# Kernel optimization log

Measured on AMD Instinct MI355X. Metric: run time of the kernel, lower is better.

Reference implementation:

```python
import jax, jax.numpy as jnp
import numpy as np

DIM = 1024
HEADS = 16
HIDDEN = 4 * DIM


def layernorm(x, g, b, eps=1e-5):
    mu = jnp.mean(x, axis=-1, keepdims=True)
    var = jnp.mean(jnp.square(x - mu), axis=-1, keepdims=True)
    return (x - mu) * jax.lax.rsqrt(var + eps) * g + b


def setup_inputs() -> dict:
    key = jax.random.key(0)
    ks = jax.random.split(key, 8)
    s = DIM ** -0.5
    return {
        "x": jax.random.normal(ks[0], (2, 2048, DIM), dtype=jnp.float32),
        "ln1_g": jnp.ones((DIM,), jnp.float32),
        "ln1_b": jnp.zeros((DIM,), jnp.float32),
        "qkv_w": jax.random.normal(ks[1], (DIM, 3 * DIM), jnp.float32) * s,
        "proj_w": jax.random.normal(ks[2], (DIM, DIM), jnp.float32) * s,
        "proj_b": jnp.zeros((DIM,), jnp.float32),
        "ln2_g": jnp.ones((DIM,), jnp.float32),
        "ln2_b": jnp.zeros((DIM,), jnp.float32),
        "fc1_w": jax.random.normal(ks[3], (DIM, HIDDEN), jnp.float32) * s,
        "fc1_b": jnp.zeros((HIDDEN,), jnp.float32),
        "fc2_w": jax.random.normal(ks[4], (HIDDEN, DIM), jnp.float32) * (HIDDEN ** -0.5),
        "fc2_b": jnp.zeros((DIM,), jnp.float32),
    }


def block_fwd(x, ln1_g, ln1_b, qkv_w, proj_w, proj_b, ln2_g, ln2_b,
              fc1_w, fc1_b, fc2_w, fc2_b):
    B, N, C = x.shape
    H = HEADS
    Dh = C // H
    scale = Dh ** -0.5
    # --- attention branch (pre-norm) ---
    h = layernorm(x, ln1_g, ln1_b)
    qkv = h @ qkv_w                     # [B,N,3C] (no bias: qkv_bias=False)
    qkv = qkv.reshape(B, N, 3, H, Dh)
    q = qkv[:, :, 0].transpose(0, 2, 1, 3)   # [B,H,N,Dh]
    k = qkv[:, :, 1].transpose(0, 2, 1, 3)
    v = qkv[:, :, 2].transpose(0, 2, 1, 3)
    attn = jnp.einsum('bhqd,bhkd->bhqk', q, k) * scale
    attn = jax.nn.softmax(attn, axis=-1)
    o = jnp.einsum('bhqk,bhkd->bhqd', attn, v)
    o = o.transpose(0, 2, 1, 3).reshape(B, N, C)
    x = x + (o @ proj_w + proj_b)
    # --- MLP branch (pre-norm) ---
    h = layernorm(x, ln2_g, ln2_b)
    h = jax.nn.gelu(h @ fc1_w + fc1_b, approximate=False)  # torch nn.GELU = exact erf
    x = x + (h @ fc2_w + fc2_b)
    return x


def reference(x, ln1_g, ln1_b, qkv_w, proj_w, proj_b, ln2_g, ln2_b,
              fc1_w, fc1_b, fc2_w, fc2_b):
    return block_fwd(x, ln1_g, ln1_b, qkv_w, proj_w, proj_b, ln2_g, ln2_b,
                     fc1_w, fc1_b, fc2_w, fc2_b)
```

## Files before the change

kernel.cpp:

```cpp
#include <hip/hip_runtime.h>
#include <math.h>

typedef unsigned short u16;
typedef unsigned int u32;
typedef __attribute__((ext_vector_type(8))) short short8;
typedef __attribute__((ext_vector_type(4))) float f32x4;
typedef __attribute__((ext_vector_type(16))) float f32x16;
typedef __attribute__((ext_vector_type(2))) u32 u32x2;
typedef __attribute__((ext_vector_type(4))) u32 u32x4;
typedef __attribute__((ext_vector_type(4))) u16 u16x4;

typedef __attribute__((address_space(1))) const void gmem_t;
typedef __attribute__((address_space(3))) void lmem_t;

__device__ __forceinline__ u16 f2bf(float f) {
  u32 u = __builtin_bit_cast(u32, f);
  u = u + 0x7fffu + ((u >> 16) & 1u);
  return (u16)(u >> 16);
}

__device__ __forceinline__ u32 cvt_pk_bf16(float a, float b) {
  u32 r;
  asm("v_cvt_pk_bf16_f32 %0, %1, %2" : "=v"(r) : "v"(a), "v"(b));
  return r;
}

__device__ __forceinline__ void g2l16(const void* g, void* l) {
  __builtin_amdgcn_global_load_lds((gmem_t*)g, (lmem_t*)l, 16, 0, 0);
}

template <int N> __device__ __forceinline__ void waitcnt_vm() {
  if constexpr (N == 0)      asm volatile("s_waitcnt vmcnt(0)" ::: "memory");
  else if constexpr (N == 4) asm volatile("s_waitcnt vmcnt(4)" ::: "memory");
  else if constexpr (N == 6) asm volatile("s_waitcnt vmcnt(6)" ::: "memory");
  else if constexpr (N == 8) asm volatile("s_waitcnt vmcnt(8)" ::: "memory");
  else static_assert(N == 0 || N == 4 || N == 6 || N == 8, "add literal");
}

#define QSCALE 0.1803368801111204f

__global__ __launch_bounds__(256) void wtrans_all(
    const float* __restrict__ qkvw, const float* __restrict__ projw,
    const float* __restrict__ fc1w, const float* __restrict__ fc2w,
    u16* __restrict__ o_qkv, u16* __restrict__ o_proj,
    u16* __restrict__ o_fc1, u16* __restrict__ o_fc2) {
  int id = (int)blockIdx.x;
  const float* in; u16* out; int R, C, bid;
  if (id < 768)       { in = qkvw;  out = o_qkv;  R = 1024; C = 3072; bid = id; }
  else if (id < 1024) { in = projw; out = o_proj; R = 1024; C = 1024; bid = id - 768; }
  else if (id < 2048) { in = fc1w;  out = o_fc1;  R = 1024; C = 4096; bid = id - 1024; }
  else                { in = fc2w;  out = o_fc2;  R = 4096; C = 1024; bid = id - 2048; }
  __shared__ float t[64][65];
  int tid = threadIdx.x;
  int nbx = C >> 6;
  int bx = bid % nbx, by = bid / nbx;
  int r0 = by << 6, c0 = bx << 6;
  int lr = tid >> 2, lc = (tid & 3) << 4;
  const float* src = in + (size_t)(r0 + lr) * C + c0 + lc;
#pragma unroll
  for (int j = 0; j < 4; ++j) {
    f32x4 v = *(const f32x4*)(src + j * 4);
    t[lr][lc + j * 4 + 0] = v.x; t[lr][lc + j * 4 + 1] = v.y;
    t[lr][lc + j * 4 + 2] = v.z; t[lr][lc + j * 4 + 3] = v.w;
  }
  __syncthreads();
  int oc = tid >> 2, orr = (tid & 3) << 4;
  u16* dst = out + (size_t)(c0 + oc) * R + r0 + orr;
  u32 u[8];
#pragma unroll
  for (int j = 0; j < 8; ++j)
    u[j] = (u32)f2bf(t[orr + 2 * j][oc]) | ((u32)f2bf(t[orr + 2 * j + 1][oc]) << 16);
  u32x4 v0; v0.x = u[0]; v0.y = u[1]; v0.z = u[2]; v0.w = u[3];
  u32x4 v1; v1.x = u[4]; v1.y = u[5]; v1.z = u[6]; v1.w = u[7];
  *(u32x4*)(dst) = v0;
  *(u32x4*)(dst + 8) = v1;
}

__global__ __launch_bounds__(256) void lnorm(const float* __restrict__ in,
                                             const float* __restrict__ gw,
                                             const float* __restrict__ bw,
                                             u16* __restrict__ out) {
  int r = blockIdx.x, tid = threadIdx.x;
  const f32x4 v = *((const f32x4*)(in + (size_t)r * 1024) + tid);
  float s = v.x + v.y + v.z + v.w;
  float ss = v.x * v.x + v.y * v.y + v.z * v.z + v.w * v.w;
#pragma unroll
  for (int o = 32; o >= 1; o >>= 1) { s += __shfl_xor(s, o); ss += __shfl_xor(ss, o); }
  __shared__ float red[8];
  int w = tid >> 6;
  if ((tid & 63) == 0) { red[w] = s; red[4 + w] = ss; }
  __syncthreads();
  s = red[0] + red[1] + red[2] + red[3];
  ss = red[4] + red[5] + red[6] + red[7];
  float mu = s * (1.0f / 1024.0f);
  float var = ss * (1.0f / 1024.0f) - mu * mu;
  float rstd = rsqrtf(var + 1e-5f);
  const f32x4 g4 = *((const f32x4*)gw + tid);
  const f32x4 b4 = *((const f32x4*)bw + tid);
  u16x4 o;
  o.x = f2bf((v.x - mu) * rstd * g4.x + b4.x);
  o.y = f2bf((v.y - mu) * rstd * g4.y + b4.y);
  o.z = f2bf((v.z - mu) * rstd * g4.z + b4.z);
  o.w = f2bf((v.w - mu) * rstd * g4.w + b4.w);
  *((u16x4*)(out + (size_t)r * 1024) + tid) = o;
}

template <int EPI, int BM, int BN>
__global__ __launch_bounds__(256, 2) void gemm_bt(
    const u16* __restrict__ A, const u16* __restrict__ BT, int M, int N, int K,
    const float* __restrict__ bias, const float* __restrict__ resid,
    float* __restrict__ fout, u16* __restrict__ bout) {
  constexpr int AIT = BM / 32, BIT = BN / 32;
  constexpr int L = AIT + BIT;
  constexpr int MR = BM / 32, NR = BN / 32;
  __shared__ __align__(16) u16 smA[2][BM * 64];
  __shared__ __align__(16) u16 smB[2][BN * 64];
  int tid = threadIdx.x;
  int w = tid >> 6, l = tid & 63, lq = l & 15, g = l >> 4;
  int nbx = N / BN;
  int t = (int)blockIdx.x;
  int cpx = (int)gridDim.x >> 3;
  t = (t & 7) * cpx + (t >> 3);
  int by = t / nbx, bx = t - by * nbx;
  long brow = (long)by * BM, bcol = (long)bx * BN;
  int wr = w >> 1, wc = w & 1;

  const u16* aS[AIT]; const u16* bS[BIT];
#pragma unroll
  for (int it = 0; it < AIT; ++it) {
    int p = it * 256 + tid;
    int row = p >> 3;
    int gc = (p & 7) ^ (row & 7);
    aS[it] = A + (size_t)(brow + row) * K + gc * 8;
  }
#pragma unroll
  for (int it = 0; it < BIT; ++it) {
    int p = it * 256 + tid;
    int row = p >> 3;
    int gc = (p & 7) ^ (row & 7);
    bS[it] = BT + (size_t)(bcol + row) * K + gc * 8;
  }
  auto STAGE = [&](int buf, int k0) {
#pragma unroll
    for (int it = 0; it < AIT; ++it) g2l16(aS[it] + k0, &smA[buf][it * 2048 + w * 512]);
#pragma unroll
    for (int it = 0; it < BIT; ++it) g2l16(bS[it] + k0, &smB[buf][it * 2048 + w * 512]);
  };

  f32x4 zero = {0.f, 0.f, 0.f, 0.f};
  f32x4 acc[MR][NR];
#pragma unroll
  for (int m = 0; m < MR; ++m)
#pragma unroll
    for (int n = 0; n < NR; ++n) acc[m][n] = zero;

  int NT = K >> 6;
  STAGE(0, 0);
  for (int tt = 0; tt < NT; ++tt) {
    int cur = tt & 1;
    int knext = ((tt + 1) == NT ? 0 : (tt + 1)) << 6;
    STAGE(cur ^ 1, knext);
    waitcnt_vm<L>();
    __builtin_amdgcn_s_barrier();
    asm volatile("" ::: "memory");

    const char* sA = (const char*)&smA[cur][0];
    const char* sB = (const char*)&smB[cur][0];
#pragma unroll
    for (int c = 0; c < 2; ++c) {
      short8 af[MR], bfb[NR];
#pragma unroll
      for (int m = 0; m < MR; ++m) {
        int r = wr * (BM / 2) + m * 16 + lq;
        af[m] = *(const short8*)(sA + r * 128 + ((g * 16 + c * 64) ^ ((r & 7) << 4)));
      }
#pragma unroll
      for (int n = 0; n < NR; ++n) {
        int r = wc * (BN / 2) + n * 16 + lq;
        bfb[n] = *(const short8*)(sB + r * 128 + ((g * 16 + c * 64) ^ ((r & 7) << 4)));
      }
#pragma unroll
      for (int m = 0; m < MR; ++m)
#pragma unroll
        for (int n = 0; n < NR; ++n)
          acc[m][n] = __builtin_amdgcn_mfma_f32_16x16x32_bf16(af[m], bfb[n], acc[m][n], 0, 0, 0);
    }
    asm volatile("" ::: "memory");
    __builtin_amdgcn_s_barrier();
  }
  waitcnt_vm<0>();

  long colbase = bcol + wc * (BN / 2);
#pragma unroll
  for (int m = 0; m < MR; ++m) {
#pragma unroll
    for (int n = 0; n < NR; ++n) {
      f32x4 v = acc[m][n];
      long col = colbase + n * 16 + lq;
      long row0 = brow + wr * (BM / 2) + m * 16 + g * 4;
      float bb = bias[col];
#pragma unroll
      for (int i = 0; i < 4; ++i) {
        long idx = (row0 + i) * N + col;
        fout[idx] = resid[idx] + v[i] + bb;
      }
    }
  }
}

template <int EPI>
__global__ __launch_bounds__(256, 4) void gemm32(
    const u16* __restrict__ A, const u16* __restrict__ BT, int M, int N, int K,
    const float* __restrict__ bias,
    u16* __restrict__ bout, u16* __restrict__ bout2, u16* __restrict__ bout3) {
  __shared__ __align__(16) u16 smA[2][128 * 32];
  __shared__ __align__(16) u16 smB[2][128 * 32];
  int tid = threadIdx.x;
  int w = tid >> 6, l = tid & 63, lq = l & 15, g = l >> 4;
  int nbx = N >> 7;
  int t = (int)blockIdx.x;
  int cpx = (int)gridDim.x >> 3;
  t = (t & 7) * cpx + (t >> 3);
  int by = t / nbx, bx = t - by * nbx;
  long brow = (long)by << 7, bcol = (long)bx << 7;
  int wr = w >> 1, wc = w & 1;

  const u16* aS[2]; const u16* bS[2];
#pragma unroll
  for (int it = 0; it < 2; ++it) {
    int p = it * 256 + tid;
    int sp = (p & 7) ^ ((p >> 3) & 7);
    int row = ((p >> 3) << 1) | (sp >> 2);
    int c = sp & 3;
    aS[it] = A + (size_t)(brow + row) * K + c * 8;
    bS[it] = BT + (size_t)(bcol + row) * K + c * 8;
  }
  auto STAGE = [&](int buf, int k0) {
#pragma unroll
    for (int it = 0; it < 2; ++it) {
      g2l16(aS[it] + k0, &smA[buf][it * 2048 + w * 512]);
      g2l16(bS[it] + k0, &smB[buf][it * 2048 + w * 512]);
    }
  };

  f32x4 zero = {0.f, 0.f, 0.f, 0.f};
  f32x4 acc[4][4];
#pragma unroll
  for (int m = 0; m < 4; ++m)
#pragma unroll
    for (int n = 0; n < 4; ++n) acc[m][n] = zero;

  int NT = K >> 5;
  STAGE(0, 0);
  for (int tt = 0; tt < NT; ++tt) {
    int cur = tt & 1;
    int knext = ((tt + 1) == NT ? 0 : (tt + 1)) << 5;
    STAGE(cur ^ 1, knext);
    waitcnt_vm<4>();
    __builtin_amdgcn_s_barrier();
    asm volatile("" ::: "memory");

    const char* sA = (const char*)&smA[cur][0];
    const char* sB = (const char*)&smB[cur][0];
    short8 af[4], bfb[4];
#pragma unroll
    for (int m = 0; m < 4; ++m) {
      int r = wr * 64 + m * 16 + lq;
      af[m] = *(const short8*)(sA + ((r >> 1) * 128 +
                ((((r & 1) << 6) + (g << 4)) ^ (((r >> 1) & 7) << 4))));
    }
#pragma unroll
    for (int n = 0; n < 4; ++n) {
      int r = wc * 64 + n * 16 + lq;
      bfb[n] = *(const short8*)(sB + ((r >> 1) * 128 +
                ((((r & 1) << 6) + (g << 4)) ^ (((r >> 1) & 7) << 4))));
    }
    __builtin_amdgcn_s_setprio(1);
#pragma unroll
    for (int m = 0; m < 4; ++m)
#pragma unroll
      for (int n = 0; n < 4; ++n)
        acc[m][n] = __builtin_amdgcn_mfma_f32_16x16x32_bf16(af[m], bfb[n], acc[m][n], 0, 0, 0);
    __builtin_amdgcn_s_setprio(0);
    asm volatile("" ::: "memory");
    __builtin_amdgcn_s_barrier();
  }
  waitcnt_vm<0>();

#pragma unroll
  for (int m = 0; m < 4; ++m) {
#pragma unroll
    for (int n = 0; n < 4; ++n) {
      f32x4 v = acc[m][n];
      long col = bcol + wc * 64 + n * 16 + lq;
      long row0 = brow + wr * 64 + m * 16 + g * 4;
      if constexpr (EPI == 0) {
        int part = (int)(bcol >> 10);
        long colq = col - ((long)part << 10);
        int hh = (int)(colq >> 6), d = (int)(colq & 63);
#pragma unroll
        for (int i = 0; i < 4; ++i) {
          long row = row0 + i;
          long b = row >> 11, nq = row & 2047;
          long bh = b * 16 + hh;
          if (part == 0)      bout [(bh * 2048 + nq) * 64 + d] = f2bf(v[i] * QSCALE);
          else if (part == 1) bout2[(bh * 2048 + nq) * 64 + d] = f2bf(v[i]);
          else                bout3[(bh * 64 + d) * 2048 + nq] = f2bf(v[i]);
        }
      } else {
        float bb = bias[col];
#pragma unroll
        for (int i = 0; i < 4; ++i) {
          float xg = v[i] + bb;
          float ge = 0.5f * xg * (1.0f + erff(xg * 0.70710678118654752f));
          bout[(row0 + i) * (long)N + col] = f2bf(ge);
        }
      }
    }
  }
}

template <int BASE>
__device__ __forceinline__ short8 mk_pfrag(const f32x16& s) {
  u32 x = cvt_pk_bf16(exp2f(s[BASE + 0]), exp2f(s[BASE + 1]));
  u32 y = cvt_pk_bf16(exp2f(s[BASE + 2]), exp2f(s[BASE + 3]));
  u32 u = cvt_pk_bf16(exp2f(s[BASE + 4]), exp2f(s[BASE + 5]));
  u32 v = cvt_pk_bf16(exp2f(s[BASE + 6]), exp2f(s[BASE + 7]));
  asm("v_permlane32_swap_b32 %0, %1" : "+v"(x), "+v"(u));
  asm("v_permlane32_swap_b32 %0, %1" : "+v"(y), "+v"(v));
  u32x4 f; f.x = x; f.y = y; f.z = u; f.w = v;
  return __builtin_bit_cast(short8, f);
}

__global__ __launch_bounds__(256, 2) void attn_fwd(const u16* __restrict__ qb,
                                                   const u16* __restrict__ kbuf,
                                                   const u16* __restrict__ vtb,
                                                   u16* __restrict__ ob) {
  __shared__ __align__(16) u16 kl[2][64 * 64];
  __shared__ __align__(16) u16 vl[2][64 * 64];
  int tid = threadIdx.x;
  int w = tid >> 6, l = tid & 63, q32 = l & 31, hi = l >> 5;
  int bh = (int)blockIdx.x & 31;
  int qt = (int)blockIdx.x >> 5;

  const u16* qp = qb + ((size_t)bh * 2048 + qt * 128 + w * 32 + q32) * 64 + hi * 8;
  short8 qf[4];
#pragma unroll
  for (int kc = 0; kc < 4; ++kc) qf[kc] = *(const short8*)(qp + kc * 16);

  const u16* kS[2]; const u16* vS[2];
#pragma unroll
  for (int it = 0; it < 2; ++it) {
    int p = it * 256 + tid;
    int row = p >> 3;
    int gc = (p & 7) ^ (row & 7);
    kS[it] = kbuf + ((size_t)bh * 2048 + row) * 64 + gc * 8;
    vS[it] = vtb + ((size_t)bh * 64 + row) * 2048 + gc * 8;
  }
  auto issue = [&](int buf, int kt0) {
#pragma unroll
    for (int it = 0; it < 2; ++it) {
      g2l16(kS[it] + (size_t)kt0 * 64, &kl[buf][it * 2048 + w * 512]);
      g2l16(vS[it] + kt0,              &vl[buf][it * 2048 + w * 512]);
    }
  };

  f32x16 z16 = {0,0,0,0,0,0,0,0,0,0,0,0,0,0,0,0};
  f32x16 accO0 = z16, accO1 = z16, accl = z16;
  u32x4 ov; ov.x = ov.y = ov.z = ov.w = 0x3F803F80u;
  short8 onesf = __builtin_bit_cast(short8, ov);
  int swz = (q32 & 7) << 4;

  issue(0, 0);
  for (int t = 0; t < 32; ++t) {
    int cur = t & 1;
    issue(cur ^ 1, ((t + 1) & 31) << 6);
    waitcnt_vm<4>();
    __builtin_amdgcn_s_barrier();
    asm volatile("" ::: "memory");

    const char* klc = (const char*)&kl[cur][0];
    const char* vlc = (const char*)&vl[cur][0];

    f32x16 s0 = z16, s1 = z16;
    __builtin_amdgcn_s_setprio(1);
#pragma unroll
    for (int kc = 0; kc < 4; ++kc) {
      short8 k0 = *(const short8*)(klc + (q32 * 128 +        ((kc * 32 + hi * 16) ^ swz)));
      short8 k1 = *(const short8*)(klc + ((32 + q32) * 128 + ((kc * 32 + hi * 16) ^ swz)));
      s0 = __builtin_amdgcn_mfma_f32_32x32x16_bf16(k0, qf[kc], s0, 0, 0, 0);
      s1 = __builtin_amdgcn_mfma_f32_32x32x16_bf16(k1, qf[kc], s1, 0, 0, 0);
    }
    __builtin_amdgcn_s_setprio(0);

    short8 pf0 = mk_pfrag<0>(s0);
    short8 pf1 = mk_pfrag<8>(s0);
    short8 pf2 = mk_pfrag<0>(s1);
    short8 pf3 = mk_pfrag<8>(s1);

    short8 va0[4], va1[4];
#pragma unroll
    for (int c = 0; c < 4; ++c) {
      va0[c] = *(const short8*)(vlc + (q32 * 128 +        ((c * 32 + hi * 16) ^ swz)));
      va1[c] = *(const short8*)(vlc + ((32 + q32) * 128 + ((c * 32 + hi * 16) ^ swz)));
    }
    __builtin_amdgcn_s_setprio(1);
    accO0 = __builtin_amdgcn_mfma_f32_32x32x16_bf16(va0[0], pf0, accO0, 0, 0, 0);
    accO1 = __builtin_amdgcn_mfma_f32_32x32x16_bf16(va1[0], pf0, accO1, 0, 0, 0);
    accl  = __builtin_amdgcn_mfma_f32_32x32x16_bf16(onesf,  pf0, accl,  0, 0, 0);
    accO0 = __builtin_amdgcn_mfma_f32_32x32x16_bf16(va0[1], pf1, accO0, 0, 0, 0);
    accO1 = __builtin_amdgcn_mfma_f32_32x32x16_bf16(va1[1], pf1, accO1, 0, 0, 0);
    accl  = __builtin_amdgcn_mfma_f32_32x32x16_bf16(onesf,  pf1, accl,  0, 0, 0);
    accO0 = __builtin_amdgcn_mfma_f32_32x32x16_bf16(va0[2], pf2, accO0, 0, 0, 0);
    accO1 = __builtin_amdgcn_mfma_f32_32x32x16_bf16(va1[2], pf2, accO1, 0, 0, 0);
    accl  = __builtin_amdgcn_mfma_f32_32x32x16_bf16(onesf,  pf2, accl,  0, 0, 0);
    accO0 = __builtin_amdgcn_mfma_f32_32x32x16_bf16(va0[3], pf3, accO0, 0, 0, 0);
    accO1 = __builtin_amdgcn_mfma_f32_32x32x16_bf16(va1[3], pf3, accO1, 0, 0, 0);
    accl  = __builtin_amdgcn_mfma_f32_32x32x16_bf16(onesf,  pf3, accl,  0, 0, 0);
    __builtin_amdgcn_s_setprio(0);

    asm volatile("" ::: "memory");
    __builtin_amdgcn_s_barrier();
  }
  waitcnt_vm<0>();

  float li = 1.0f / accl[0];
  int b = bh >> 4, h = bh & 15;
  long q = (long)qt * 128 + w * 32 + q32;
  u16* obase = ob + ((long)b * 2048 + q) * 1024 + h * 64;
#pragma unroll
  for (int j = 0; j < 8; ++j) {
    int d = ((2 * j) & 3) + 8 * (j >> 1) + 4 * hi;
    *(u32*)(obase + d)      = cvt_pk_bf16(accO0[2 * j] * li, accO0[2 * j + 1] * li);
    *(u32*)(obase + 32 + d) = cvt_pk_bf16(accO1[2 * j] * li, accO1[2 * j + 1] * li);
  }
}

extern "C" void kernel_launch(void* const* d_in, const int* in_sizes, int n_in,
                              void* d_out, int out_size, void* d_ws, size_t ws_size,
                              hipStream_t stream) {
  const float* x     = (const float*)d_in[0];
  const float* ln1g  = (const float*)d_in[1];
  const float* ln1b  = (const float*)d_in[2];
  const float* qkvw  = (const float*)d_in[3];
  const float* projw = (const float*)d_in[4];
  const float* projb = (const float*)d_in[5];
  const float* ln2g  = (const float*)d_in[6];
  const float* ln2b  = (const float*)d_in[7];
  const float* fc1w  = (const float*)d_in[8];
  const float* fc1b  = (const float*)d_in[9];
  const float* fc2w  = (const float*)d_in[10];
  const float* fc2b  = (const float*)d_in[11];
  char* ws = (char*)d_ws;
  u16* qkv_wt  = (u16*)(ws + 0);
  u16* proj_wt = (u16*)(ws + 6291456);
  u16* fc1_wt  = (u16*)(ws + 8388608);
  u16* fc2_wt  = (u16*)(ws + 16777216);
  u16* h       = (u16*)(ws + 25165824);
  u16* qbuf    = (u16*)(ws + 33554432);
  u16* kbuf    = (u16*)(ws + 41943040);
  u16* vtbuf   = (u16*)(ws + 50331648);
  u16* aout    = (u16*)(ws + 58720256);
  float* y1    = (float*)(ws + 67108864);
  u16* gbuf    = (u16*)(ws + 33554432);
  float* outp  = (float*)d_out;

  wtrans_all<<<3072, 256, 0, stream>>>(qkvw, projw, fc1w, fc2w,
                                       qkv_wt, proj_wt, fc1_wt, fc2_wt);

  lnorm<<<4096, 256, 0, stream>>>(x, ln1g, ln1b, h);
  gemm32<0><<<768, 256, 0, stream>>>(h, qkv_wt, 4096, 3072, 1024,
                                     nullptr, qbuf, kbuf, vtbuf);
  attn_fwd<<<512, 256, 0, stream>>>(qbuf, kbuf, vtbuf, aout);
  gemm_bt<1, 64, 128><<<512, 256, 0, stream>>>(aout, proj_wt, 4096, 1024, 1024,
                                               projb, x, y1, nullptr);
  lnorm<<<4096, 256, 0, stream>>>(y1, ln2g, ln2b, h);
  gemm32<2><<<1024, 256, 0, stream>>>(h, fc1_wt, 4096, 4096, 1024,
                                      fc1b, gbuf, nullptr, nullptr);
  gemm_bt<3, 64, 128><<<512, 256, 0, stream>>>(gbuf, fc2_wt, 4096, 1024, 4096,
                                               fc2b, y1, outp, nullptr);
}
```

Measured before the change: 243.9 us.

## Add 256x256-tile 512-thread GEMM kernel for FC1 with fused GELU

Adds a dedicated GEMM kernel for the FC1 projection that uses 256x256 output tiles per 8-wave workgroup with double-buffered, swizzled LDS staging and a fused bias+erf-GELU epilogue. It replaces the previous gemm32 launch that used 1024 smaller blocks. The larger tile increases operand reuse per LDS load and reduces global traffic. In exchange it uses many more accumulator registers and launches only 256 workgroups, which may limit occupancy and load balance across CUs.

```diff
diff --git a/kernel.cpp b/kernel.cpp
--- a/kernel.cpp
+++ b/kernel.cpp
@@ -315,6 +315,99 @@
           float ge = 0.5f * xg * (1.0f + erff(xg * 0.70710678118654752f));
           bout[(row0 + i) * (long)N + col] = f2bf(ge);
         }
+      }
+    }
+  }
+}
+
+__global__ __launch_bounds__(512, 2) void gemm256(
+    const u16* __restrict__ A, const u16* __restrict__ BT, int M, int N, int K,
+    const float* __restrict__ bias, u16* __restrict__ bout) {
+  __shared__ __align__(16) u16 smA[2][256 * 32];
+  __shared__ __align__(16) u16 smB[2][256 * 32];
+  int tid = threadIdx.x;
+  int w = tid >> 6, l = tid & 63, lq = l & 15, g = l >> 4;
+  int nbx = N >> 8;
+  int t = (int)blockIdx.x;
+  int cpx = (int)gridDim.x >> 3;
+  t = (t & 7) * cpx + (t >> 3);
+  int by = t / nbx, bx = t - by * nbx;
+  long brow = (long)by << 8, bcol = (long)bx << 8;
+  int wr = w >> 2, wc = w & 3;
+
+  const u16* aS[2]; const u16* bS[2];
+#pragma unroll
+  for (int it = 0; it < 2; ++it) {
+    int p = it * 512 + tid;
+    int sp = (p & 7) ^ ((p >> 3) & 7);
+    int row = ((p >> 3) << 1) | (sp >> 2);
+    int c = sp & 3;
+    aS[it] = A + (size_t)(brow + row) * K + c * 8;
+    bS[it] = BT + (size_t)(bcol + row) * K + c * 8;
+  }
+  auto STAGE = [&](int buf, int k0) {
+#pragma unroll
+    for (int it = 0; it < 2; ++it) {
+      g2l16(aS[it] + k0, &smA[buf][it * 4096 + w * 512]);
+      g2l16(bS[it] + k0, &smB[buf][it * 4096 + w * 512]);
+    }
+  };
+
+  f32x4 zero = {0.f, 0.f, 0.f, 0.f};
+  f32x4 acc[8][4];
+#pragma unroll
+  for (int m = 0; m < 8; ++m)
+#pragma unroll
+    for (int n = 0; n < 4; ++n) acc[m][n] = zero;
+
+  int NT = K >> 5;
+  STAGE(0, 0);
+  STAGE(1, 32);
+  for (int tt = 0; tt < NT; ++tt) {
+    if (tt == NT - 1) waitcnt_vm<0>(); else waitcnt_vm<4>();
+    __builtin_amdgcn_s_barrier();
+    asm volatile("" ::: "memory");
+
+    const char* sA = (const char*)&smA[tt & 1][0];
+    const char* sB = (const char*)&smB[tt & 1][0];
+    short8 af[8], bfb[4];
+#pragma unroll
+    for (int m = 0; m < 8; ++m) {
+      int r = wr * 128 + m * 16 + lq;
+      af[m] = *(const short8*)(sA + ((r >> 1) * 128 +
+                ((((r & 1) << 6) + (g << 4)) ^ (((r >> 1) & 7) << 4))));
+    }
+#pragma unroll
+    for (int n = 0; n < 4; ++n) {
+      int r = wc * 64 + n * 16 + lq;
+      bfb[n] = *(const short8*)(sB + ((r >> 1) * 128 +
+                ((((r & 1) << 6) + (g << 4)) ^ (((r >> 1) & 7) << 4))));
+    }
+    __builtin_amdgcn_s_setprio(1);
+#pragma unroll
+    for (int m = 0; m < 8; ++m)
+#pragma unroll
+      for (int n = 0; n < 4; ++n)
+        acc[m][n] = __builtin_amdgcn_mfma_f32_16x16x32_bf16(af[m], bfb[n], acc[m][n], 0, 0, 0);
+    __builtin_amdgcn_s_setprio(0);
+    asm volatile("" ::: "memory");
+    __builtin_amdgcn_s_barrier();
+    if (tt + 2 < NT) STAGE(tt & 1, (tt + 2) << 5);
+  }
+
+#pragma unroll
+  for (int m = 0; m < 8; ++m) {
+#pragma unroll
+    for (int n = 0; n < 4; ++n) {
+      f32x4 v = acc[m][n];
+      long col = bcol + wc * 64 + n * 16 + lq;
+      long row0 = brow + wr * 128 + m * 16 + g * 4;
+      float bb = bias[col];
+#pragma unroll
+      for (int i = 0; i < 4; ++i) {
+        float xg = v[i] + bb;
+        float ge = 0.5f * xg * (1.0f + erff(xg * 0.70710678118654752f));
+        bout[(row0 + i) * (long)N + col] = f2bf(ge);
       }
     }
   }
@@ -475,8 +568,7 @@
   gemm_bt<1, 64, 128><<<512, 256, 0, stream>>>(aout, proj_wt, 4096, 1024, 1024,
                                                projb, x, y1, nullptr);
   lnorm<<<4096, 256, 0, stream>>>(y1, ln2g, ln2b, h);
-  gemm32<2><<<1024, 256, 0, stream>>>(h, fc1_wt, 4096, 4096, 1024,
-                                      fc1b, gbuf, nullptr, nullptr);
+  gemm256<<<256, 512, 0, stream>>>(h, fc1_wt, 4096, 4096, 1024, fc1b, gbuf);
   gemm_bt<3, 64, 128><<<512, 256, 0, stream>>>(gbuf, fc2_wt, 4096, 1024, 4096,
                                                fc2b, y1, outp, nullptr);
 }
```

New measurement: 251.3 us. +3.0%, slower.
